# Performance work log

Measured on AMD Instinct MI355X. Metric: run time of the kernel, lower is better.

## Reference

```python
import jax, jax.numpy as jnp
import numpy as np

N = 100_000   # num nodes
E = 1_600_000 # num edges
C = 128       # in_channels == hidden_channels
L = 3         # n_layers
EPS = 1e-5    # BatchNorm eps (torch default)


def bn(h, g, b, m, v):
    # BatchNorm1d in eval mode: running stats
    return (h - m) * jax.lax.rsqrt(v + EPS) * g + b


def sage_layer(h, src, dst, Wl_i, bl_i, Wr_i):
    # mean aggregation of incoming neighbor messages (PyG SAGEConv default)
    msg = h[src]                                                   # [E, C] gather
    agg = jax.ops.segment_sum(msg, dst, num_segments=N)            # [N, C]
    cnt = jax.ops.segment_sum(jnp.ones((src.shape[0],), h.dtype), dst, num_segments=N)
    agg = agg / jnp.maximum(cnt, 1.0)[:, None]
    return agg @ Wl_i + bl_i + h @ Wr_i                            # lin_l(agg) + lin_r(x)


def setup_inputs() -> dict:
    key = jax.random.key(0)
    ks = jax.random.split(key, 32)
    s = 0.05
    d = {}
    d["x"] = jax.random.normal(ks[0], (N, C), jnp.float32)
    d["edge_index"] = jax.random.randint(ks[1], (2, E), 0, N, dtype=jnp.int32)
    d["batch_size"] = 50_000
    d["Wl"] = jax.random.normal(ks[2], (L, C, C), jnp.float32) * s
    d["bl"] = jax.random.normal(ks[3], (L, C), jnp.float32) * s
    d["Wr"] = jax.random.normal(ks[4], (L, C, C), jnp.float32) * s
    d["bn_g"] = jax.random.uniform(ks[5], (L, C), jnp.float32, 0.5, 1.5)
    d["bn_b"] = jax.random.normal(ks[6], (L, C), jnp.float32) * s
    d["bn_m"] = jax.random.normal(ks[7], (L, C), jnp.float32) * s
    d["bn_v"] = jax.random.uniform(ks[8], (L, C), jnp.float32, 0.5, 1.5)
    d["cW1"] = jax.random.normal(ks[9], (C, C), jnp.float32) * s
    d["cb1"] = jax.random.normal(ks[10], (C,), jnp.float32) * s
    d["cg1"] = jax.random.uniform(ks[11], (C,), jnp.float32, 0.5, 1.5)
    d["cbe1"] = jax.random.normal(ks[12], (C,), jnp.float32) * s
    d["cm1"] = jax.random.normal(ks[13], (C,), jnp.float32) * s
    d["cv1"] = jax.random.uniform(ks[14], (C,), jnp.float32, 0.5, 1.5)
    d["cW2"] = jax.random.normal(ks[15], (C, C // 2), jnp.float32) * s
    d["cb2"] = jax.random.normal(ks[16], (C // 2,), jnp.float32) * s
    d["cg2"] = jax.random.uniform(ks[17], (C // 2,), jnp.float32, 0.5, 1.5)
    d["cbe2"] = jax.random.normal(ks[18], (C // 2,), jnp.float32) * s
    d["cm2"] = jax.random.normal(ks[19], (C // 2,), jnp.float32) * s
    d["cv2"] = jax.random.uniform(ks[20], (C // 2,), jnp.float32, 0.5, 1.5)
    d["cW3"] = jax.random.normal(ks[21], (C // 2, 1), jnp.float32) * s
    d["cb3"] = jax.random.normal(ks[22], (1,), jnp.float32) * s
    return d


def reference(x, edge_index, batch_size, Wl, bl, Wr, bn_g, bn_b, bn_m, bn_v,
              cW1, cb1, cg1, cbe1, cm1, cv1,
              cW2, cb2, cg2, cbe2, cm2, cv2, cW3, cb3):
    src, dst = edge_index[0], edge_index[1]
    h = x
    for l in range(L):  # small fixed layer count
        h = bn(jax.nn.relu(sage_layer(h, src, dst, Wl[l], bl[l], Wr[l])),
               bn_g[l], bn_b[l], bn_m[l], bn_v[l])
        # dropout is identity in eval mode
    h = h[:batch_size]                                             # [B, C] seed nodes
    h = jax.nn.relu(bn(h @ cW1 + cb1, cg1, cbe1, cm1, cv1))
    h = jax.nn.relu(bn(h @ cW2 + cb2, cg2, cbe2, cm2, cv2))
    return (h @ cW3 + cb3)[:, 0]                                   # [B]
```

## Files before the change

### kernel.cpp

```cpp
#include <hip/hip_runtime.h>

#define N_NODES 100000
#define N_EDGES 1600000
#define CDIM    128
#define BATCH   50000
#define NLAYERS 3
#define EPS_BN  1e-5f
#define LPAD    136

#define NBUCK   512
#define BW      196
#define EPB     4096
#define NEB     ((N_EDGES + EPB - 1) / EPB)
#define EBCAP   3584

#define ECAP    704

typedef __attribute__((ext_vector_type(8))) short short8;
typedef __attribute__((ext_vector_type(4))) float floatx4;
typedef __attribute__((ext_vector_type(2))) float floatx2;

__device__ __forceinline__ unsigned short f2bf(float f) {
    unsigned int u = __float_as_uint(f);
    u = u + 0x7FFFu + ((u >> 16) & 1u);
    return (unsigned short)(u >> 16);
}
__device__ __forceinline__ void unpk(unsigned int u, float& lo, float& hi) {
    lo = __uint_as_float(u << 16);
    hi = __uint_as_float(u & 0xFFFF0000u);
}
__device__ __forceinline__ unsigned int pk2(float lo, float hi) {
    return (unsigned int)f2bf(lo) | ((unsigned int)f2bf(hi) << 16);
}

__device__ __forceinline__ void accp0(uint4 u, floatx2& a01, floatx2& a23,
                                      floatx2& a45, floatx2& a67) {
    floatx2 v;
    v.x = __uint_as_float(u.x << 16); v.y = __uint_as_float(u.x & 0xFFFF0000u);
    a01 = a01 + v;
    v.x = __uint_as_float(u.y << 16); v.y = __uint_as_float(u.y & 0xFFFF0000u);
    a23 = a23 + v;
    v.x = __uint_as_float(u.z << 16); v.y = __uint_as_float(u.z & 0xFFFF0000u);
    a45 = a45 + v;
    v.x = __uint_as_float(u.w << 16); v.y = __uint_as_float(u.w & 0xFFFF0000u);
    a67 = a67 + v;
}
__device__ __forceinline__ void accpw(uint4 u, float w, floatx2& a01, floatx2& a23,
                                      floatx2& a45, floatx2& a67) {
    floatx2 wv; wv.x = w; wv.y = w;
    floatx2 v;
    v.x = __uint_as_float(u.x << 16); v.y = __uint_as_float(u.x & 0xFFFF0000u);
    a01 = v * wv + a01;
    v.x = __uint_as_float(u.y << 16); v.y = __uint_as_float(u.y & 0xFFFF0000u);
    a23 = v * wv + a23;
    v.x = __uint_as_float(u.z << 16); v.y = __uint_as_float(u.z & 0xFFFF0000u);
    a45 = v * wv + a45;
    v.x = __uint_as_float(u.w << 16); v.y = __uint_as_float(u.w & 0xFFFF0000u);
    a67 = v * wv + a67;
}

#define OFF_HB0   6400000
#define OFF_HB1   12800000
#define OFF_SC    19200000
#define OFF_RP    19201152
#define OFF_BCNT  19301184
#define OFF_ELIST 19302752
#define OFF_EBUF  20902752
#define OFF_WCAT  22737760
#define OFF_WH1   22786912
#define OFF_WH2   22795104

#define XBLK 12500
#define WBLK 384
#define HBLK 96
__global__ __launch_bounds__(256) void setup_all(
        const float* __restrict__ x,
        const float* __restrict__ Wl, const float* __restrict__ Wr,
        const float* __restrict__ cW1, const float* __restrict__ cW2,
        const float* __restrict__ g, const float* __restrict__ b,
        const float* __restrict__ m, const float* __restrict__ v,
        const float* __restrict__ cg1, const float* __restrict__ cbe1,
        const float* __restrict__ cm1, const float* __restrict__ cv1,
        const float* __restrict__ cg2, const float* __restrict__ cbe2,
        const float* __restrict__ cm2, const float* __restrict__ cv2,
        float* __restrict__ ws) {
    int blk = blockIdx.x;
    int tid = threadIdx.x;
    unsigned short* xb = (unsigned short*)ws;

    if (blk < XBLK) {
        int i = blk * 256 + tid;
        float4 vv = ((const float4*)x)[i];
        ushort4 o;
        o.x = f2bf(vv.x); o.y = f2bf(vv.y); o.z = f2bf(vv.z); o.w = f2bf(vv.w);
        ((ushort4*)xb)[i] = o;
        return;
    }
    if (blk < XBLK + WBLK) {
        unsigned short* wcat = (unsigned short*)(ws + OFF_WCAT);
        int i = (blk - XBLK) * 256 + tid;
        int l = i >> 15;
        int n = (i >> 8) & 127;
        int k = i & 255;
        float w = (k < CDIM) ? Wl[((size_t)l * CDIM + k) * CDIM + n]
                             : Wr[((size_t)l * CDIM + (k - CDIM)) * CDIM + n];
        wcat[i] = f2bf(w);
        return;
    }
    if (blk < XBLK + WBLK + HBLK) {
        unsigned short* wh1 = (unsigned short*)(ws + OFF_WH1);
        unsigned short* wh2 = (unsigned short*)(ws + OFF_WH2);
        int i = (blk - XBLK - WBLK) * 256 + tid;
        if (i < 128 * 128) {
            int n = i >> 7, k = i & 127;
            wh1[i] = f2bf(cW1[k * 128 + n]);
        } else if (i < 128 * 128 + 64 * 128) {
            int j = i - 128 * 128;
            int n = j >> 7, k = j & 127;
            wh2[j] = f2bf(cW2[k * 64 + n]);
        }
        return;
    }
    float* sc = ws + OFF_SC;
    int* bcnt = (int*)(ws + OFF_BCNT);
    for (int i = tid; i < NLAYERS * CDIM; i += 256) {
        float s = g[i] * rsqrtf(v[i] + EPS_BN);
        sc[i] = s;
        sc[NLAYERS * CDIM + i] = b[i] - m[i] * s;
    }
    if (tid < CDIM) {
        float s = cg1[tid] * rsqrtf(cv1[tid] + EPS_BN);
        sc[768 + tid] = s;
        sc[896 + tid] = cbe1[tid] - cm1[tid] * s;
    }
    if (tid < 64) {
        float s = cg2[tid] * rsqrtf(cv2[tid] + EPS_BN);
        sc[1024 + tid] = s;
        sc[1088 + tid] = cbe2[tid] - cm2[tid] * s;
    }
    for (int i = tid; i < NBUCK; i += 256) bcnt[i] = 0;
}

__global__ __launch_bounds__(256) void bucket_fill(const int* __restrict__ ei,
                                                   int* __restrict__ bcnt,
                                                   unsigned int* __restrict__ ebuf) {
    __shared__ unsigned int st[EPB];
    __shared__ unsigned short sb[EPB];
    __shared__ int lh[NBUCK];
    __shared__ int gb[NBUCK];
    __shared__ int lc[NBUCK];
    int tid = threadIdx.x;
    for (int t = tid; t < NBUCK; t += 256) { lh[t] = 0; lc[t] = 0; }
    __syncthreads();
    int base = blockIdx.x * EPB;
    int cnt = min(EPB, N_EDGES - base);
    for (int k = tid; k < cnt / 4; k += 256) {
        int4 s4 = ((const int4*)(ei + base))[k];
        int4 d4 = ((const int4*)(ei + N_EDGES + base))[k];
        int i0 = k * 4;
#pragma unroll
        for (int q = 0; q < 4; ++q) {
            int s = (q == 0) ? s4.x : (q == 1) ? s4.y : (q == 2) ? s4.z : s4.w;
            int d = (q == 0) ? d4.x : (q == 1) ? d4.y : (q == 2) ? d4.z : d4.w;
            int bk = (unsigned)d / BW;
            int ld = d - bk * BW;
            st[i0 + q] = (unsigned)s | ((unsigned)ld << 17);
            sb[i0 + q] = (unsigned short)bk;
            atomicAdd(&lh[bk], 1);
        }
    }
    __syncthreads();
    for (int t = tid; t < NBUCK; t += 256) {
        int c = lh[t];
        gb[t] = c ? (t * EBCAP + atomicAdd(&bcnt[t], c)) : 0;
    }
    __syncthreads();
    for (int i = tid; i < cnt; i += 256) {
        int bk = sb[i];
        int pos = gb[bk] + atomicAdd(&lc[bk], 1);
        ebuf[pos] = st[i];
    }
}

__global__ __launch_bounds__(256) void bucket_csr(const unsigned int* __restrict__ ebuf,
                                                  const int* __restrict__ bcnt,
                                                  int* __restrict__ elist,
                                                  int* __restrict__ rowptr) {
    __shared__ int sbb[NBUCK];
    __shared__ unsigned int st[EBCAP];
    __shared__ int out[EBCAP];
    __shared__ int h[256], sscan[256], pre[256], cur[256];
    int b = blockIdx.x;
    int tid = threadIdx.x;
    int cnt = min(bcnt[b], EBCAP);

    sbb[tid] = bcnt[tid];
    sbb[tid + 256] = bcnt[tid + 256];
    h[tid] = 0; cur[tid] = 0;
    __syncthreads();
    for (int off = 1; off < NBUCK; off <<= 1) {
        int v0 = (tid >= off) ? sbb[tid - off] : 0;
        int t2 = tid + 256;
        int v1 = sbb[t2 - off];
        __syncthreads();
        sbb[tid] += v0;
        sbb[t2] += v1;
        __syncthreads();
    }
    int obase = (b == 0) ? 0 : sbb[b - 1];

    int ebase = b * EBCAP;
    for (int i = tid; i < cnt; i += 256) {
        unsigned int u = ebuf[ebase + i];
        st[i] = u;
        atomicAdd(&h[u >> 17], 1);
    }
    __syncthreads();
    sscan[tid] = h[tid];
    __syncthreads();
    for (int off = 1; off < 256; off <<= 1) {
        int v = (tid >= off) ? sscan[tid - off] : 0;
        __syncthreads();
        sscan[tid] += v;
        __syncthreads();
    }
    pre[tid] = sscan[tid] - h[tid];
    __syncthreads();
    for (int i = tid; i < cnt; i += 256) {
        unsigned int u = st[i];
        int ld = u >> 17;
        int pos = pre[ld] + atomicAdd(&cur[ld], 1);
        out[pos] = (int)(u & 0x1FFFFu);
    }
    __syncthreads();
    for (int i = tid; i < cnt; i += 256) elist[obase + i] = out[i];
    int gn = b * BW + tid;
    if (tid < BW && gn < N_NODES) rowptr[gn] = obase + pre[tid];
    if (b == 0 && tid == 0) rowptr[N_NODES] = N_EDGES;
}

__global__ __launch_bounds__(256, 6) void sage_fused(const int* __restrict__ rowptr,
                                                     const int* __restrict__ elist,
                                                     const unsigned short* __restrict__ hin,
                                                     unsigned short* __restrict__ hout,
                                                     const unsigned short* __restrict__ wcat,
                                                     const float* __restrict__ bl,
                                                     const float* __restrict__ scale,
                                                     const float* __restrict__ shift) {
    __shared__ unsigned short sA[32][LPAD];
    __shared__ unsigned short sH[32][LPAD];
    __shared__ int selist[ECAP + 8];
    __shared__ int srp[33];

    int row0 = blockIdx.x * 32;
    int tid = threadIdx.x;
    int lane = tid & 31;
    int grp = tid >> 5;
    int sub = lane >> 4;
    int li  = lane & 15;
    int li8 = li * 8;

    int beg0 = rowptr[row0];
    int end0 = rowptr[row0 + 32];
    int ecnt = min(end0 - beg0, ECAP);
    for (int i = tid; i < ecnt + 8; i += 256)
        selist[i] = (i < ecnt) ? elist[beg0 + i] : 0;
    if (tid < 33) srp[tid] = rowptr[row0 + tid];
    for (int it = 0; it < 4; ++it) {
        int idx = it * 256 + tid;
        int r = idx >> 5;
        int c4 = idx & 31;
        uint2 u = ((const uint2*)(hin + (size_t)(row0 + r) * CDIM))[c4];
        *((uint2*)&sH[r][c4 * 4]) = u;
    }
    __syncthreads();

    for (int rr = 0; rr < 4; ++rr) {
        int r = rr * 8 + grp;
        int beg = srp[r];
        int end = srp[r + 1];
        bool all_cached = (end - beg0) <= ecnt;
        floatx2 a01 = (floatx2)0.f, a23 = (floatx2)0.f,
                a45 = (floatx2)0.f, a67 = (floatx2)0.f;

        for (int j = beg + sub * 8; j < end; j += 16) {
            int lj = j - beg0;
            int s0, s1, s2, s3, s4, s5, s6, s7;
            if (all_cached || (lj + 8 <= ecnt)) {
                s0 = selist[lj];     s1 = selist[lj + 1];
                s2 = selist[lj + 2]; s3 = selist[lj + 3];
                s4 = selist[lj + 4]; s5 = selist[lj + 5];
                s6 = selist[lj + 6]; s7 = selist[lj + 7];
            } else {
                s0 = elist[j];     s1 = elist[j + 1];
                s2 = elist[j + 2]; s3 = elist[j + 3];
                s4 = elist[j + 4]; s5 = elist[j + 5];
                s6 = elist[j + 6]; s7 = elist[j + 7];
            }
            bool p1 = (j + 1 < end), p2 = (j + 2 < end), p3 = (j + 3 < end),
                 p4 = (j + 4 < end), p5 = (j + 5 < end), p6 = (j + 6 < end),
                 p7 = (j + 7 < end);
            s1 = p1 ? s1 : 0; s2 = p2 ? s2 : 0; s3 = p3 ? s3 : 0;
            s4 = p4 ? s4 : 0; s5 = p5 ? s5 : 0; s6 = p6 ? s6 : 0;
            s7 = p7 ? s7 : 0;
            uint4 u0 = *((const uint4*)(hin + (unsigned)((s0 << 7) + li8)));
            uint4 u1 = *((const uint4*)(hin + (unsigned)((s1 << 7) + li8)));
            uint4 u2 = *((const uint4*)(hin + (unsigned)((s2 << 7) + li8)));
            uint4 u3 = *((const uint4*)(hin + (unsigned)((s3 << 7) + li8)));
            uint4 u4 = *((const uint4*)(hin + (unsigned)((s4 << 7) + li8)));
            uint4 u5 = *((const uint4*)(hin + (unsigned)((s5 << 7) + li8)));
            uint4 u6 = *((const uint4*)(hin + (unsigned)((s6 << 7) + li8)));
            uint4 u7 = *((const uint4*)(hin + (unsigned)((s7 << 7) + li8)));
            accp0(u0, a01, a23, a45, a67);
            accpw(u1, p1 ? 1.f : 0.f, a01, a23, a45, a67);
            accpw(u2, p2 ? 1.f : 0.f, a01, a23, a45, a67);
            accpw(u3, p3 ? 1.f : 0.f, a01, a23, a45, a67);
            accpw(u4, p4 ? 1.f : 0.f, a01, a23, a45, a67);
            accpw(u5, p5 ? 1.f : 0.f, a01, a23, a45, a67);
            accpw(u6, p6 ? 1.f : 0.f, a01, a23, a45, a67);
            accpw(u7, p7 ? 1.f : 0.f, a01, a23, a45, a67);
        }

        float a0 = a01.x, a1 = a01.y, a2 = a23.x, a3 = a23.y,
              a4 = a45.x, a5 = a45.y, a6 = a67.x, a7 = a67.y;
        a0 += __shfl_xor(a0, 16); a1 += __shfl_xor(a1, 16);
        a2 += __shfl_xor(a2, 16); a3 += __shfl_xor(a3, 16);
        a4 += __shfl_xor(a4, 16); a5 += __shfl_xor(a5, 16);
        a6 += __shfl_xor(a6, 16); a7 += __shfl_xor(a7, 16);
        if (sub == 0) {
            float rin = 1.0f / fmaxf((float)(end - beg), 1.0f);
            uint4 o;
            o.x = pk2(a0 * rin, a1 * rin);
            o.y = pk2(a2 * rin, a3 * rin);
            o.z = pk2(a4 * rin, a5 * rin);
            o.w = pk2(a6 * rin, a7 * rin);
            *((uint4*)&sA[r][li8]) = o;
        }
    }
    __syncthreads();

    int wave = tid >> 6;
    int wl   = tid & 63;
    int ln16 = wl & 15;
    int quad = wl >> 4;

    floatx4 acc[2][2];
#pragma unroll
    for (int mt = 0; mt < 2; ++mt)
#pragma unroll
        for (int nt = 0; nt < 2; ++nt) acc[mt][nt] = (floatx4)0.0f;

    const unsigned short* wbase = wcat + ((size_t)(wave * 32 + ln16) * 256 + quad * 8);

#pragma unroll
    for (int kb = 0; kb < 8; ++kb) {
        int koff = (kb & 3) * 32 + quad * 8;
        const unsigned short* sbuf = (kb < 4) ? &sA[0][0] : &sH[0][0];
        short8 a0 = *((const short8*)(sbuf + (ln16)      * LPAD + koff));
        short8 a1 = *((const short8*)(sbuf + (ln16 + 16) * LPAD + koff));
        short8 b0 = *((const short8*)(wbase + kb * 32));
        short8 b1 = *((const short8*)(wbase + 16 * 256 + kb * 32));
        acc[0][0] = __builtin_amdgcn_mfma_f32_16x16x32_bf16(a0, b0, acc[0][0], 0, 0, 0);
        acc[1][0] = __builtin_amdgcn_mfma_f32_16x16x32_bf16(a1, b0, acc[1][0], 0, 0, 0);
        acc[0][1] = __builtin_amdgcn_mfma_f32_16x16x32_bf16(a0, b1, acc[0][1], 0, 0, 0);
        acc[1][1] = __builtin_amdgcn_mfma_f32_16x16x32_bf16(a1, b1, acc[1][1], 0, 0, 0);
    }

    __syncthreads();
#pragma unroll
    for (int nt = 0; nt < 2; ++nt) {
        int col = wave * 32 + nt * 16 + ln16;
        float bb = bl[col];
        float ss = scale[col];
        float tt = shift[col];
#pragma unroll
        for (int mt = 0; mt < 2; ++mt) {
#pragma unroll
            for (int r = 0; r < 4; ++r) {
                float v = fmaxf(acc[mt][nt][r] + bb, 0.0f) * ss + tt;
                sA[mt * 16 + quad * 4 + r][col] = f2bf(v);
            }
        }
    }
    __syncthreads();
#pragma unroll
    for (int it = 0; it < 2; ++it) {
        int idx = it * 256 + tid;
        int r = idx >> 4;
        int c = idx & 15;
        uint4 u = *((const uint4*)&sA[r][c * 8]);
        *((uint4*)(hout + (size_t)(row0 + r) * CDIM + c * 8)) = u;
    }
}

__global__ __launch_bounds__(256, 4) void head_fused(const unsigned short* __restrict__ hin,
                                                     const unsigned short* __restrict__ wh1,
                                                     const unsigned short* __restrict__ wh2,
                                                     const float* __restrict__ cb1,
                                                     const float* __restrict__ s1,
                                                     const float* __restrict__ t1,
                                                     const float* __restrict__ cb2,
                                                     const float* __restrict__ s2,
                                                     const float* __restrict__ t2,
                                                     const float* __restrict__ W3,
                                                     const float* __restrict__ b3,
                                                     float* __restrict__ out) {
    __shared__ unsigned short sZ[64][LPAD];
    __shared__ float sP[4][64];
    __shared__ float sw3[64];

    int row0 = blockIdx.x * 64;
    int tid = threadIdx.x;
    if (tid < 64) sw3[tid] = W3[tid];

    for (int it = 0; it < 4; ++it) {
        int idx = it * 256 + tid;
        int r = idx >> 4;
        int c = idx & 15;
        uint4 u = *((const uint4*)(hin + (size_t)(row0 + r) * CDIM + c * 8));
        *((uint4*)&sZ[r][c * 8]) = u;
    }
    __syncthreads();

    int wave = tid >> 6;
    int wl   = tid & 63;
    int ln16 = wl & 15;
    int quad = wl >> 4;

    floatx4 a1[4][2];
#pragma unroll
    for (int mt = 0; mt < 4; ++mt) { a1[mt][0] = (floatx4)0.0f; a1[mt][1] = (floatx4)0.0f; }

    const unsigned short* w1a = wh1 + (size_t)(wave * 32 + ln16) * 128 + quad * 8;
    const unsigned short* w1b = w1a + 16 * 128;

#pragma unroll
    for (int kb = 0; kb < 4; ++kb) {
        int koff = kb * 32 + quad * 8;
        short8 b0 = *((const short8*)(w1a + kb * 32));
        short8 b1 = *((const short8*)(w1b + kb * 32));
#pragma unroll
        for (int mt = 0; mt < 4; ++mt) {
            short8 af = *((const short8*)(&sZ[mt * 16 + ln16][koff]));
            a1[mt][0] = __builtin_amdgcn_mfma_f32_16x16x32_bf16(af, b0, a1[mt][0], 0, 0, 0);
            a1[mt][1] = __builtin_amdgcn_mfma_f32_16x16x32_bf16(af, b1, a1[mt][1], 0, 0, 0);
        }
    }

    __syncthreads();
#pragma unroll
    for (int nt = 0; nt < 2; ++nt) {
        int col = wave * 32 + nt * 16 + ln16;
        float bb = cb1[col], ss = s1[col], tt = t1[col];
#pragma unroll
        for (int mt = 0; mt < 4; ++mt) {
#pragma unroll
            for (int r = 0; r < 4; ++r) {
                float v = fmaxf((a1[mt][nt][r] + bb) * ss + tt, 0.0f);
                sZ[mt * 16 + quad * 4 + r][col] = f2bf(v);
            }
        }
    }
    __syncthreads();

    floatx4 a2[4];
#pragma unroll
    for (int mt = 0; mt < 4; ++mt) a2[mt] = (floatx4)0.0f;

    const unsigned short* w2a = wh2 + (size_t)(wave * 16 + ln16) * 128 + quad * 8;

#pragma unroll
    for (int kb = 0; kb < 4; ++kb) {
        int koff = kb * 32 + quad * 8;
        short8 b0 = *((const short8*)(w2a + kb * 32));
#pragma unroll
        for (int mt = 0; mt < 4; ++mt) {
            short8 af = *((const short8*)(&sZ[mt * 16 + ln16][koff]));
            a2[mt] = __builtin_amdgcn_mfma_f32_16x16x32_bf16(af, b0, a2[mt], 0, 0, 0);
        }
    }

    {
        int col = wave * 16 + ln16;
        float bb = cb2[col], ss = s2[col], tt = t2[col];
        float w3v = sw3[col];
#pragma unroll
        for (int mt = 0; mt < 4; ++mt) {
#pragma unroll
            for (int r = 0; r < 4; ++r) {
                float v = fmaxf((a2[mt][r] + bb) * ss + tt, 0.0f) * w3v;
                v += __shfl_xor(v, 1);
                v += __shfl_xor(v, 2);
                v += __shfl_xor(v, 4);
                v += __shfl_xor(v, 8);
                if (ln16 == 0) sP[wave][mt * 16 + quad * 4 + r] = v;
            }
        }
    }
    __syncthreads();
    if (tid < 64) {
        int row = row0 + tid;
        if (row < BATCH)
            out[row] = sP[0][tid] + sP[1][tid] + sP[2][tid] + sP[3][tid] + b3[0];
    }
}

extern "C" void kernel_launch(void* const* d_in, const int* in_sizes, int n_in,
                              void* d_out, int out_size, void* d_ws, size_t ws_size,
                              hipStream_t stream) {
    const float* x    = (const float*)d_in[0];
    const int*   ei   = (const int*)d_in[1];
    const float* Wl   = (const float*)d_in[3];
    const float* bl   = (const float*)d_in[4];
    const float* Wr   = (const float*)d_in[5];
    const float* bn_g = (const float*)d_in[6];
    const float* bn_b = (const float*)d_in[7];
    const float* bn_m = (const float*)d_in[8];
    const float* bn_v = (const float*)d_in[9];
    const float* cW1  = (const float*)d_in[10];
    const float* cb1  = (const float*)d_in[11];
    const float* cg1  = (const float*)d_in[12];
    const float* cbe1 = (const float*)d_in[13];
    const float* cm1  = (const float*)d_in[14];
    const float* cv1  = (const float*)d_in[15];
    const float* cW2  = (const float*)d_in[16];
    const float* cb2  = (const float*)d_in[17];
    const float* cg2  = (const float*)d_in[18];
    const float* cbe2 = (const float*)d_in[19];
    const float* cm2  = (const float*)d_in[20];
    const float* cv2  = (const float*)d_in[21];
    const float* cW3  = (const float*)d_in[22];
    const float* cb3  = (const float*)d_in[23];

    float* ws  = (float*)d_ws;
    unsigned short* xb  = (unsigned short*)ws;
    unsigned short* hb0 = (unsigned short*)(ws + OFF_HB0);
    unsigned short* hb1 = (unsigned short*)(ws + OFF_HB1);
    float* sc    = ws + OFF_SC;
    int* rowptr  = (int*)(ws + OFF_RP);
    int* bcnt    = (int*)(ws + OFF_BCNT);
    int* elist   = (int*)(ws + OFF_ELIST);
    unsigned int* ebuf = (unsigned int*)(ws + OFF_EBUF);
    unsigned short* wcat = (unsigned short*)(ws + OFF_WCAT);
    unsigned short* wh1  = (unsigned short*)(ws + OFF_WH1);
    unsigned short* wh2  = (unsigned short*)(ws + OFF_WH2);

    setup_all<<<XBLK + WBLK + HBLK + 1, 256, 0, stream>>>(
        x, Wl, Wr, cW1, cW2,
        bn_g, bn_b, bn_m, bn_v,
        cg1, cbe1, cm1, cv1,
        cg2, cbe2, cm2, cv2, ws);

    bucket_fill<<<NEB, 256, 0, stream>>>(ei, bcnt, ebuf);
    bucket_csr<<<NBUCK, 256, 0, stream>>>(ebuf, bcnt, elist, rowptr);

    const unsigned short* lin[NLAYERS] = { xb, hb0, hb1 };
    unsigned short* lout[NLAYERS]      = { hb0, hb1, hb0 };
    for (int l = 0; l < NLAYERS; ++l) {
        sage_fused<<<N_NODES / 32, 256, 0, stream>>>(
            rowptr, elist, lin[l], lout[l],
            wcat + (size_t)l * CDIM * 256,
            bl + (size_t)l * CDIM,
            sc + l * CDIM, sc + 384 + l * CDIM);
    }

    head_fused<<<(BATCH + 63) / 64, 256, 0, stream>>>(
        hb0, wh1, wh2,
        cb1, sc + 768, sc + 896,
        cb2, sc + 1024, sc + 1088,
        cW3, cb3, (float*)d_out);
}
```

Measured before the change: 384.8 us.

## Merge setup and bucket fill kernels, limit last layer to seed nodes

Folds the edge bucketing into the setup kernel as extra blocks and replaces the in-kernel bcnt zeroing with a memset issued before it. This removes one launch and lets the conversion and bucketing work overlap. The last SAGE layer now runs only over the first BATCH nodes, because the head reads only those rows, which roughly halves that layer's work. Merging adds the bucketing kernel's large shared-memory footprint to every setup block, which may lower occupancy for the simple conversion blocks.

```diff
diff --git a/kernel.cpp b/kernel.cpp
--- a/kernel.cpp
+++ b/kernel.cpp
@@ -16,6 +16,8 @@
 
 #define ECAP    704
 
+#define BBLK3   ((BATCH + 31) / 32)
+
 typedef __attribute__((ext_vector_type(8))) short short8;
 typedef __attribute__((ext_vector_type(4))) float floatx4;
 typedef __attribute__((ext_vector_type(2))) float floatx2;
@@ -24,10 +26,6 @@
     unsigned int u = __float_as_uint(f);
     u = u + 0x7FFFu + ((u >> 16) & 1u);
     return (unsigned short)(u >> 16);
-}
-__device__ __forceinline__ void unpk(unsigned int u, float& lo, float& hi) {
-    lo = __uint_as_float(u << 16);
-    hi = __uint_as_float(u & 0xFFFF0000u);
 }
 __device__ __forceinline__ unsigned int pk2(float lo, float hi) {
     return (unsigned int)f2bf(lo) | ((unsigned int)f2bf(hi) << 16);
@@ -73,7 +71,8 @@
 #define XBLK 12500
 #define WBLK 384
 #define HBLK 96
-__global__ __launch_bounds__(256) void setup_all(
+#define SETUP_BLKS (XBLK + WBLK + HBLK + 1)
+__global__ __launch_bounds__(256) void setup_fill(
         const float* __restrict__ x,
         const float* __restrict__ Wl, const float* __restrict__ Wr,
         const float* __restrict__ cW1, const float* __restrict__ cW2,
@@ -83,7 +82,16 @@
         const float* __restrict__ cm1, const float* __restrict__ cv1,
         const float* __restrict__ cg2, const float* __restrict__ cbe2,
         const float* __restrict__ cm2, const float* __restrict__ cv2,
+        const int* __restrict__ ei,
+        int* __restrict__ bcnt,
+        unsigned int* __restrict__ ebuf,
         float* __restrict__ ws) {
+    __shared__ unsigned int st[EPB];
+    __shared__ unsigned short sb[EPB];
+    __shared__ int lh[NBUCK];
+    __shared__ int gb[NBUCK];
+    __shared__ int lc[NBUCK];
+
     int blk = blockIdx.x;
     int tid = threadIdx.x;
     unsigned short* xb = (unsigned short*)ws;
@@ -121,38 +129,30 @@
         }
         return;
     }
-    float* sc = ws + OFF_SC;
-    int* bcnt = (int*)(ws + OFF_BCNT);
-    for (int i = tid; i < NLAYERS * CDIM; i += 256) {
-        float s = g[i] * rsqrtf(v[i] + EPS_BN);
-        sc[i] = s;
-        sc[NLAYERS * CDIM + i] = b[i] - m[i] * s;
-    }
-    if (tid < CDIM) {
-        float s = cg1[tid] * rsqrtf(cv1[tid] + EPS_BN);
-        sc[768 + tid] = s;
-        sc[896 + tid] = cbe1[tid] - cm1[tid] * s;
-    }
-    if (tid < 64) {
-        float s = cg2[tid] * rsqrtf(cv2[tid] + EPS_BN);
-        sc[1024 + tid] = s;
-        sc[1088 + tid] = cbe2[tid] - cm2[tid] * s;
-    }
-    for (int i = tid; i < NBUCK; i += 256) bcnt[i] = 0;
-}
-
-__global__ __launch_bounds__(256) void bucket_fill(const int* __restrict__ ei,
-                                                   int* __restrict__ bcnt,
-                                                   unsigned int* __restrict__ ebuf) {
-    __shared__ unsigned int st[EPB];
-    __shared__ unsigned short sb[EPB];
-    __shared__ int lh[NBUCK];
-    __shared__ int gb[NBUCK];
-    __shared__ int lc[NBUCK];
-    int tid = threadIdx.x;
+    if (blk == XBLK + WBLK + HBLK) {
+        float* sc = ws + OFF_SC;
+        for (int i = tid; i < NLAYERS * CDIM; i += 256) {
+            float s = g[i] * rsqrtf(v[i] + EPS_BN);
+            sc[i] = s;
+            sc[NLAYERS * CDIM + i] = b[i] - m[i] * s;
+        }
+        if (tid < CDIM) {
+            float s = cg1[tid] * rsqrtf(cv1[tid] + EPS_BN);
+            sc[768 + tid] = s;
+            sc[896 + tid] = cbe1[tid] - cm1[tid] * s;
+        }
+        if (tid < 64) {
+            float s = cg2[tid] * rsqrtf(cv2[tid] + EPS_BN);
+            sc[1024 + tid] = s;
+            sc[1088 + tid] = cbe2[tid] - cm2[tid] * s;
+        }
+        return;
+    }
+
+    int fb = blk - SETUP_BLKS;
     for (int t = tid; t < NBUCK; t += 256) { lh[t] = 0; lc[t] = 0; }
     __syncthreads();
-    int base = blockIdx.x * EPB;
+    int base = fb * EPB;
     int cnt = min(EPB, N_EDGES - base);
     for (int k = tid; k < cnt / 4; k += 256) {
         int4 s4 = ((const int4*)(ei + base))[k];
@@ -545,19 +545,22 @@
     unsigned short* wh1  = (unsigned short*)(ws + OFF_WH1);
     unsigned short* wh2  = (unsigned short*)(ws + OFF_WH2);
 
-    setup_all<<<XBLK + WBLK + HBLK + 1, 256, 0, stream>>>(
+    hipMemsetAsync(bcnt, 0, NBUCK * sizeof(int), stream);
+
+    setup_fill<<<SETUP_BLKS + NEB, 256, 0, stream>>>(
         x, Wl, Wr, cW1, cW2,
         bn_g, bn_b, bn_m, bn_v,
         cg1, cbe1, cm1, cv1,
-        cg2, cbe2, cm2, cv2, ws);
-
-    bucket_fill<<<NEB, 256, 0, stream>>>(ei, bcnt, ebuf);
+        cg2, cbe2, cm2, cv2,
+        ei, bcnt, ebuf, ws);
+
     bucket_csr<<<NBUCK, 256, 0, stream>>>(ebuf, bcnt, elist, rowptr);
 
     const unsigned short* lin[NLAYERS] = { xb, hb0, hb1 };
     unsigned short* lout[NLAYERS]      = { hb0, hb1, hb0 };
+    int grids[NLAYERS] = { N_NODES / 32, N_NODES / 32, BBLK3 };
     for (int l = 0; l < NLAYERS; ++l) {
-        sage_fused<<<N_NODES / 32, 256, 0, stream>>>(
+        sage_fused<<<grids[l], 256, 0, stream>>>(
             rowptr, elist, lin[l], lout[l],
             wcat + (size_t)l * CDIM * 256,
             bl + (size_t)l * CDIM,
```

After: 363.1 us. 1.06x faster.
